# Kernel optimization log

Hardware: AMD Instinct MI355X
Metric: run time of the kernel (lower is better)

## Reference

```python
import jax, jax.numpy as jnp
import numpy as np

V, E, H, B, S = 50000, 512, 1024, 256, 256


def setup_inputs() -> dict:
    key = jax.random.key(0)
    ks = jax.random.split(key, 8)
    inputs = jax.random.randint(ks[0], (B, S), 0, V)
    emb = jax.random.normal(ks[1], (V, E), dtype=jnp.float32)
    sx, sh = 1.0 / np.sqrt(E), 1.0 / np.sqrt(H)  # ~orthogonal column scale
    Wx_f = jax.random.normal(ks[2], (E, 4 * H), dtype=jnp.float32) * sx
    Wh_f = jax.random.normal(ks[3], (H, 4 * H), dtype=jnp.float32) * sh
    Wx_b = jax.random.normal(ks[4], (E, 4 * H), dtype=jnp.float32) * sx
    Wh_b = jax.random.normal(ks[5], (H, 4 * H), dtype=jnp.float32) * sh
    # gate order i, f, o, c ; forget-gate bias initialized to 1 as in the source
    bias = jnp.concatenate([jnp.zeros(H), jnp.ones(H), jnp.zeros(H), jnp.zeros(H)]).astype(jnp.float32)
    W_hq = jax.random.normal(ks[6], (H, 10), dtype=jnp.float32) * sh
    b_q = jnp.zeros(10, dtype=jnp.float32)
    return {"inputs": inputs, "emb": emb, "Wx_f": Wx_f, "Wh_f": Wh_f, "b_f": bias,
            "Wx_b": Wx_b, "Wh_b": Wh_b, "b_b": bias, "W_hq": W_hq, "b_q": b_q}


def _lstm_final_h(x_tbe, Wx, Wh, b):
    """x_tbe: [S,B,E] time-major. Returns final hidden state [B,H]."""
    h0 = jnp.zeros((x_tbe.shape[1], H), dtype=x_tbe.dtype)
    c0 = jnp.zeros_like(h0)

    def cell(carry, X):
        h, c = carry
        g = X @ Wx + h @ Wh + b          # [B, 4H] fused gate pre-activations
        i, f, o, ct = jnp.split(g, 4, axis=-1)
        c = jax.nn.sigmoid(f) * c + jax.nn.sigmoid(i) * jnp.tanh(ct)
        h = jax.nn.sigmoid(o) * jnp.tanh(c)
        return (h, c), None

    (h, _), _ = jax.lax.scan(cell, (h0, c0), x_tbe)
    return h


def reference(inputs, emb, Wx_f, Wh_f, b_f, Wx_b, Wh_b, b_b, W_hq, b_q):
    x = emb[inputs]                      # [B,S,E]
    x = jnp.transpose(x, (1, 0, 2))      # [S,B,E] time-major
    h_fwd = _lstm_final_h(x, Wx_f, Wh_f, b_f)
    h_bwd = _lstm_final_h(x[::-1], Wx_b, Wh_b, b_b)
    logits = (h_fwd + h_bwd) @ W_hq + b_q
    return jax.nn.softmax(logits, axis=1)
```

## Files before the change

kernel.cpp:

```cpp
#include <hip/hip_runtime.h>

#define S_LEN 256
#define BATCH 256
#define EDIM 512
#define HDIM 1024
#define LDS_BYTES 131072

typedef short short8 __attribute__((ext_vector_type(8)));
typedef float f32x4 __attribute__((ext_vector_type(4)));
typedef unsigned long long u64;
typedef unsigned short us;

__device__ __forceinline__ us f2bf(float f) {
  unsigned u = __float_as_uint(f);
  u = u + 0x7FFFu + ((u >> 16) & 1u);
  return (us)(u >> 16);
}
__device__ __forceinline__ float bf2f(us s) {
  return __uint_as_float(((unsigned)s) << 16);
}
__device__ __forceinline__ float sigf(float x) { return 1.0f / (1.0f + __expf(-x)); }
__device__ __forceinline__ float tanh_(float x) { return 2.0f / (1.0f + __expf(-2.0f * x)) - 1.0f; }

#define MFMA(d, a, b) d = __builtin_amdgcn_mfma_f32_16x16x32_bf16(a, b, d, 0, 0, 0)

__device__ __forceinline__ short8 load_hfrag(const us* p) {
  union { u64 d[2]; short8 v; } u;
  u.d[0] = __hip_atomic_load((const u64*)p,       __ATOMIC_RELAXED, __HIP_MEMORY_SCOPE_AGENT);
  u.d[1] = __hip_atomic_load((const u64*)(p + 4), __ATOMIC_RELAXED, __HIP_MEMORY_SCOPE_AGENT);
  return u.v;
}
__device__ __forceinline__ short8 ldf(const us* p) {
  union { uint4 d; short8 v; } u;
  u.d = *(const uint4*)p;
  return u.v;
}


__global__ void gather_embed(const int* __restrict__ inputs, const float* __restrict__ emb,
                             us* __restrict__ Xf) {
  int T = blockIdx.x * 256 + threadIdx.x;
  int kt = T & 15;
  int b  = (T >> 4) & 255;
  int s  = T >> 12;
  int vid = inputs[b * S_LEN + s];
  const float* src = emb + (size_t)vid * EDIM + kt * 32;
  int c = b & 15;
  us* ub = Xf + ((size_t)(s * 16 + kt) * 16 + (b >> 4)) * 512;
#pragma unroll
  for (int q = 0; q < 4; ++q) {
    float4 v0 = *(const float4*)(src + q * 8);
    float4 v1 = *(const float4*)(src + q * 8 + 4);
    us o[8] = { f2bf(v0.x), f2bf(v0.y), f2bf(v0.z), f2bf(v0.w),
                f2bf(v1.x), f2bf(v1.y), f2bf(v1.z), f2bf(v1.w) };
    *(uint4*)(ub + (size_t)(c + 16 * q) * 8) = *(const uint4*)o;
  }
}

__global__ void pack_w(const float* __restrict__ Wx_f, const float* __restrict__ Wh_f,
                       const float* __restrict__ Wx_b, const float* __restrict__ Wh_b,
                       us* __restrict__ Wxp, us* __restrict__ Whp) {
  int T = blockIdx.x * 256 + threadIdx.x;
  int c = T & 15;
  int q = (T >> 4) & 3;
  int t = (T >> 6) & 7;
  int r = T >> 9;
  int kit = r % 48;
  int jbd = r / 48;
  int jb  = jbd & 31;
  int dir = jbd >> 5;
  int g = t >> 1, h16 = t & 1;
  int n = g * 1024 + jb * 32 + h16 * 16 + c;
  const float* W; int k0;
  if (kit < 16) { W = dir ? Wx_b : Wx_f; k0 = kit * 32 + q * 8; }
  else          { W = dir ? Wh_b : Wh_f; k0 = (kit - 16) * 32 + q * 8; }
  us o[8];
#pragma unroll
  for (int e = 0; e < 8; ++e) o[e] = f2bf(W[(size_t)(k0 + e) * 4096 + n]);
  us* dst;
  if (kit < 16) dst = Wxp + (((size_t)(dir * 32 + jb) * 16 + kit) * 8 + t) * 512;
  else          dst = Whp + (((size_t)(dir * 32 + jb) * 32 + (kit - 16)) * 8 + t) * 512;
  *(uint4*)(dst + (size_t)(c + 16 * q) * 8) = *(const uint4*)o;
}

__global__ __launch_bounds__(512, 1) void lstm_main(
    const us* __restrict__ Xf,
    const us* __restrict__ Wxp,
    const us* __restrict__ Whp,
    const float* __restrict__ bias_f,
    const float* __restrict__ bias_b,
    us* __restrict__ Hf,
    unsigned int* __restrict__ slots)
{
  extern __shared__ __align__(16) unsigned char smem[];

  const int bx   = blockIdx.x;
  const int xcd  = bx & 7;
  const int dir  = xcd >> 2;
  const int joct = xcd & 3;
  const int rr   = bx >> 3;
  const int jb   = joct * 8 + (rr & 7);
  const int mq   = rr >> 3;

  const int tid  = threadIdx.x;
  const int wave = tid >> 6;
  const int lane = tid & 63;
  const int mw   = wave & 3;
  const int nw   = wave >> 2;
  const int c    = lane & 15;
  const int q    = lane >> 4;
  const int lofs = lane * 8;

  {
    const uint4* src = (const uint4*)(Whp + (((size_t)(dir * 32 + jb) * 32 + 16) * 8) * 512);
    for (int i = tid; i < 8192; i += 512) *(uint4*)(smem + (size_t)i * 16) = src[i];
  }
  const float* bias = dir ? bias_b : bias_f;
  const int j = jb * 32 + nw * 16 + c;
  float bg[4];
#pragma unroll
  for (int g = 0; g < 4; ++g) bg[g] = bias[g * HDIM + j];
  __syncthreads();

  unsigned int* grp_slots = slots + (dir * 4 + mq) * (32 * 16);
  unsigned int* my_slot   = grp_slots + jb * 16;

  const int bt0 = mq * 4 + mw;
  const us* xu_base  = Xf + (size_t)bt0 * 512 + lofs;
  const us* wxu = Wxp + (((size_t)(dir * 32 + jb) * 16) * 8 + nw) * 512 + lofs;
  const us* whu = Whp + (((size_t)(dir * 32 + jb) * 32) * 8 + nw) * 512 + lofs;
  const int ldsofs = (nw * 512 + lane * 8) * 2;

  float c_reg[4] = {0.f, 0.f, 0.f, 0.f};

  for (int s = 0; s < S_LEN; ++s) {
    const int sx = dir ? (S_LEN - 1 - s) : s;
    const int p  = s & 1;

    f32x4 acc[4];
#pragma unroll
    for (int g = 0; g < 4; ++g)
      acc[g] = (f32x4){bg[g], bg[g], bg[g], bg[g]};

    {
      const us* xu = xu_base + (size_t)sx * (16 * 16 * 512);
#pragma unroll 4
      for (int k = 0; k < 16; ++k) {
        short8 a0 = ldf(xu + (size_t)k * 8192);
        const us* wb = wxu + (size_t)k * 4096;
        short8 b0 = ldf(wb);
        short8 b1 = ldf(wb + 1024);
        short8 b2 = ldf(wb + 2048);
        short8 b3 = ldf(wb + 3072);
        MFMA(acc[0], a0, b0); MFMA(acc[1], a0, b1);
        MFMA(acc[2], a0, b2); MFMA(acc[3], a0, b3);
      }
    }

    if (s > 0) {
      if (tid < 32) {
        const unsigned int* sl = grp_slots + tid * 16;
        for (;;) {
          unsigned v = __hip_atomic_load(sl, __ATOMIC_RELAXED, __HIP_MEMORY_SCOPE_AGENT);
          if (!__any(v < (unsigned)s)) break;
          __builtin_amdgcn_s_sleep(1);
        }
      }
      __syncthreads();
      asm volatile("" ::: "memory");
    }

    {
      const us* hu = Hf + (((size_t)(p * 2 + dir) * 32) * 16 + bt0) * 512 + lofs;
      short8 pa[4];
#pragma unroll
      for (int i = 0; i < 4; ++i) pa[i] = load_hfrag(hu + (size_t)i * 8192);
#pragma unroll 4
      for (int k = 0; k < 16; ++k) {
        short8 a0 = pa[k & 3];
        pa[k & 3] = load_hfrag(hu + (size_t)(k + 4) * 8192);
        const us* wb = whu + (size_t)k * 4096;
        short8 b0 = ldf(wb);
        short8 b1 = ldf(wb + 1024);
        short8 b2 = ldf(wb + 2048);
        short8 b3 = ldf(wb + 3072);
        MFMA(acc[0], a0, b0); MFMA(acc[1], a0, b1);
        MFMA(acc[2], a0, b2); MFMA(acc[3], a0, b3);
      }
#pragma unroll 4
      for (int k = 16; k < 28; ++k) {
        short8 a0 = pa[k & 3];
        pa[k & 3] = load_hfrag(hu + (size_t)(k + 4) * 8192);
        const unsigned char* lb = smem + (size_t)(k - 16) * 8192 + ldsofs;
        short8 b0 = *(const short8*)(lb);
        short8 b1 = *(const short8*)(lb + 2048);
        short8 b2 = *(const short8*)(lb + 4096);
        short8 b3 = *(const short8*)(lb + 6144);
        MFMA(acc[0], a0, b0); MFMA(acc[1], a0, b1);
        MFMA(acc[2], a0, b2); MFMA(acc[3], a0, b3);
      }
#pragma unroll
      for (int k = 28; k < 32; ++k) {
        short8 a0 = pa[k & 3];
        const unsigned char* lb = smem + (size_t)(k - 16) * 8192 + ldsofs;
        short8 b0 = *(const short8*)(lb);
        short8 b1 = *(const short8*)(lb + 2048);
        short8 b2 = *(const short8*)(lb + 4096);
        short8 b3 = *(const short8*)(lb + 6144);
        MFMA(acc[0], a0, b0); MFMA(acc[1], a0, b1);
        MFMA(acc[2], a0, b2); MFMA(acc[3], a0, b3);
      }
    }

    {
      const int q2 = nw * 2 + (c >> 3);
      const int e2 = c & 7;
      const size_t ob = ((size_t)(((p ^ 1) * 2 + dir) * 32 + jb) * 16 + bt0) * 512;
      us* hd = Hf + ob + (size_t)(16 * q2) * 8 + e2;
#pragma unroll
      for (int rg = 0; rg < 4; ++rg) {
        float gi = acc[0][rg], gf = acc[1][rg];
        float go = acc[2][rg], gc = acc[3][rg];
        float cn = sigf(gf) * c_reg[rg] + sigf(gi) * tanh_(gc);
        c_reg[rg] = cn;
        __hip_atomic_store(hd + (size_t)(q * 4 + rg) * 8, f2bf(sigf(go) * tanh_(cn)),
                           __ATOMIC_RELAXED, __HIP_MEMORY_SCOPE_AGENT);
      }
    }
    asm volatile("s_waitcnt vmcnt(0)" ::: "memory");
    __syncthreads();
    if (tid == 0)
      __hip_atomic_store(my_slot, (unsigned)(s + 1), __ATOMIC_RELAXED, __HIP_MEMORY_SCOPE_AGENT);
  }
}

__global__ void final_softmax(const us* __restrict__ Hf,
                              const float* __restrict__ Whq,
                              const float* __restrict__ bq,
                              float* __restrict__ out) {
  __shared__ float red[4][10];
  const int b = blockIdx.x;
  const int tid = threadIdx.x;
  float acc[10];
#pragma unroll
  for (int qq = 0; qq < 10; ++qq) acc[qq] = 0.f;
#pragma unroll
  for (int u = 0; u < 4; ++u) {
    int j = tid * 4 + u;
    int kt = j >> 5, q2 = (j & 31) >> 3, e = j & 7;
    size_t idx = (((size_t)kt * 16 + (b >> 4)) * 512) + ((size_t)((b & 15) + 16 * q2)) * 8 + e;
    float xv = bf2f(Hf[idx]) + bf2f(Hf[(size_t)32 * 16 * 512 + idx]);
#pragma unroll
    for (int qq = 0; qq < 10; ++qq) acc[qq] += xv * Whq[j * 10 + qq];
  }
#pragma unroll
  for (int qq = 0; qq < 10; ++qq)
#pragma unroll
    for (int off = 32; off; off >>= 1) acc[qq] += __shfl_down(acc[qq], off, 64);
  if ((tid & 63) == 0)
#pragma unroll
    for (int qq = 0; qq < 10; ++qq) red[tid >> 6][qq] = acc[qq];
  __syncthreads();
  if (tid == 0) {
    float t[10];
#pragma unroll
    for (int qq = 0; qq < 10; ++qq)
      t[qq] = red[0][qq] + red[1][qq] + red[2][qq] + red[3][qq] + bq[qq];
    float mx = t[0];
#pragma unroll
    for (int qq = 1; qq < 10; ++qq) mx = fmaxf(mx, t[qq]);
    float sum = 0.f;
#pragma unroll
    for (int qq = 0; qq < 10; ++qq) { t[qq] = __expf(t[qq] - mx); sum += t[qq]; }
    float inv = 1.0f / sum;
#pragma unroll
    for (int qq = 0; qq < 10; ++qq) out[b * 10 + qq] = t[qq] * inv;
  }
}

extern "C" void kernel_launch(void* const* d_in, const int* in_sizes, int n_in,
                              void* d_out, int out_size, void* d_ws, size_t ws_size,
                              hipStream_t stream) {
  const int*   inputs = (const int*)d_in[0];
  const float* emb    = (const float*)d_in[1];
  const float* Wx_f   = (const float*)d_in[2];
  const float* Wh_f   = (const float*)d_in[3];
  const float* b_f    = (const float*)d_in[4];
  const float* Wx_b   = (const float*)d_in[5];
  const float* Wh_b   = (const float*)d_in[6];
  const float* b_b    = (const float*)d_in[7];
  const float* W_hq   = (const float*)d_in[8];
  const float* b_q    = (const float*)d_in[9];
  float* out = (float*)d_out;

  char* ws = (char*)d_ws;
  us* Xf  = (us*)ws;
  us* Wxp = (us*)(ws + (64ull << 20));
  us* Whp = (us*)(ws + (72ull << 20));
  us* Hf  = (us*)(ws + (88ull << 20));
  unsigned int* slt = (unsigned int*)(ws + (90ull << 20));

  hipMemsetAsync(Hf, 0, (size_t)2 * 2 * 32 * 16 * 512 * sizeof(us), stream);
  hipMemsetAsync(slt, 0, 8 * 32 * 16 * sizeof(unsigned int), stream);

  gather_embed<<<4096, 256, 0, stream>>>(inputs, emb, Xf);
  pack_w<<<6144, 256, 0, stream>>>(Wx_f, Wh_f, Wx_b, Wh_b, Wxp, Whp);

  hipFuncSetAttribute((const void*)lstm_main,
                      hipFuncAttributeMaxDynamicSharedMemorySize, LDS_BYTES);

  const us* xf_p = Xf;
  const us* wxp_p = Wxp;
  const us* whp_p = Whp;
  const float* bf_p = b_f;
  const float* bb_p = b_b;
  us* hf_p = Hf;
  unsigned int* slt_p = slt;
  void* kargs[] = { (void*)&xf_p, (void*)&wxp_p, (void*)&whp_p, (void*)&bf_p,
                    (void*)&bb_p, (void*)&hf_p, (void*)&slt_p };
  hipLaunchCooperativeKernel((void*)lstm_main, dim3(256), dim3(512), kargs, LDS_BYTES, stream);

  final_softmax<<<256, 256, 0, stream>>>(Hf, W_hq, b_q, out);
}
```

Measured before the change: 4.714 ms.

## Repartition LSTM blocks so each block's whole recurrent weight slice fits in LDS

Result: no change. 4.714 ms (-0.0%).

```diff
diff --git a/kernel.cpp b/kernel.cpp
--- a/kernel.cpp
+++ b/kernel.cpp
@@ -94,42 +94,44 @@
 {
   extern __shared__ __align__(16) unsigned char smem[];
 
-  const int bx   = blockIdx.x;
-  const int xcd  = bx & 7;
-  const int dir  = xcd >> 2;
-  const int joct = xcd & 3;
-  const int rr   = bx >> 3;
-  const int jb   = joct * 8 + (rr & 7);
-  const int mq   = rr >> 3;
+  const int bx  = blockIdx.x;
+  const int dir = bx & 1;
+  const int mq  = (bx >> 1) & 1;
+  const int J   = bx >> 2;
+  const int jh  = J & 1;
+  const int jt  = J >> 1;
 
   const int tid  = threadIdx.x;
   const int wave = tid >> 6;
   const int lane = tid & 63;
-  const int mw   = wave & 3;
-  const int nw   = wave >> 2;
   const int c    = lane & 15;
   const int q    = lane >> 4;
   const int lofs = lane * 8;
 
   {
-    const uint4* src = (const uint4*)(Whp + (((size_t)(dir * 32 + jb) * 32 + 16) * 8) * 512);
-    for (int i = tid; i < 8192; i += 512) *(uint4*)(smem + (size_t)i * 16) = src[i];
+    const uint4* W4 = (const uint4*)Whp;
+    for (int i = tid; i < 8192; i += 512) {
+      int within = i & 63;
+      int g  = (i >> 6) & 3;
+      int hk = i >> 8;
+      size_t src = ((((size_t)(dir * 32 + jt) * 32 + hk) * 8) + (g * 2 + jh)) * 64 + within;
+      *(uint4*)(smem + (size_t)i * 16) = W4[src];
+    }
   }
   const float* bias = dir ? bias_b : bias_f;
-  const int j = jb * 32 + nw * 16 + c;
+  const int j = J * 16 + c;
   float bg[4];
 #pragma unroll
   for (int g = 0; g < 4; ++g) bg[g] = bias[g * HDIM + j];
   __syncthreads();
 
-  unsigned int* grp_slots = slots + (dir * 4 + mq) * (32 * 16);
-  unsigned int* my_slot   = grp_slots + jb * 16;
-
-  const int bt0 = mq * 4 + mw;
-  const us* xu_base  = Xf + (size_t)bt0 * 512 + lofs;
-  const us* wxu = Wxp + (((size_t)(dir * 32 + jb) * 16) * 8 + nw) * 512 + lofs;
-  const us* whu = Whp + (((size_t)(dir * 32 + jb) * 32) * 8 + nw) * 512 + lofs;
-  const int ldsofs = (nw * 512 + lane * 8) * 2;
+  unsigned int* grp_slots = slots + (dir * 2 + mq) * (64 * 16);
+  unsigned int* my_slot   = grp_slots + J * 16;
+
+  const int bt0 = mq * 8 + wave;
+  const us* xu_base = Xf + (size_t)bt0 * 512 + lofs;
+  const us* wxu = Wxp + ((size_t)(dir * 32 + jt) * 16) * 8 * 512 + (size_t)jh * 512 + lofs;
+  const unsigned char* lbbase = smem + (size_t)lane * 16;
 
   float c_reg[4] = {0.f, 0.f, 0.f, 0.f};
 
@@ -158,7 +160,7 @@
     }
 
     if (s > 0) {
-      if (tid < 32) {
+      if (tid < 64) {
         const unsigned int* sl = grp_slots + tid * 16;
         for (;;) {
           unsigned v = __hip_atomic_load(sl, __ATOMIC_RELAXED, __HIP_MEMORY_SCOPE_AGENT);
@@ -176,46 +178,34 @@
 #pragma unroll
       for (int i = 0; i < 4; ++i) pa[i] = load_hfrag(hu + (size_t)i * 8192);
 #pragma unroll 4
-      for (int k = 0; k < 16; ++k) {
+      for (int k = 0; k < 28; ++k) {
         short8 a0 = pa[k & 3];
         pa[k & 3] = load_hfrag(hu + (size_t)(k + 4) * 8192);
-        const us* wb = whu + (size_t)k * 4096;
-        short8 b0 = ldf(wb);
-        short8 b1 = ldf(wb + 1024);
-        short8 b2 = ldf(wb + 2048);
-        short8 b3 = ldf(wb + 3072);
+        const unsigned char* lb = lbbase + (size_t)k * 4096;
+        short8 b0 = *(const short8*)(lb);
+        short8 b1 = *(const short8*)(lb + 1024);
+        short8 b2 = *(const short8*)(lb + 2048);
+        short8 b3 = *(const short8*)(lb + 3072);
         MFMA(acc[0], a0, b0); MFMA(acc[1], a0, b1);
         MFMA(acc[2], a0, b2); MFMA(acc[3], a0, b3);
       }
-#pragma unroll 4
-      for (int k = 16; k < 28; ++k) {
+#pragma unroll
+      for (int k = 28; k < 32; ++k) {
         short8 a0 = pa[k & 3];
-        pa[k & 3] = load_hfrag(hu + (size_t)(k + 4) * 8192);
-        const unsigned char* lb = smem + (size_t)(k - 16) * 8192 + ldsofs;
+        const unsigned char* lb = lbbase + (size_t)k * 4096;
         short8 b0 = *(const short8*)(lb);
-        short8 b1 = *(const short8*)(lb + 2048);
-        short8 b2 = *(const short8*)(lb + 4096);
-        short8 b3 = *(const short8*)(lb + 6144);
+        short8 b1 = *(const short8*)(lb + 1024);
+        short8 b2 = *(const short8*)(lb + 2048);
+        short8 b3 = *(const short8*)(lb + 3072);
         MFMA(acc[0], a0, b0); MFMA(acc[1], a0, b1);
         MFMA(acc[2], a0, b2); MFMA(acc[3], a0, b3);
       }
-#pragma unroll
-      for (int k = 28; k < 32; ++k) {
-        short8 a0 = pa[k & 3];
-        const unsigned char* lb = smem + (size_t)(k - 16) * 8192 + ldsofs;
-        short8 b0 = *(const short8*)(lb);
-        short8 b1 = *(const short8*)(lb + 2048);
-        short8 b2 = *(const short8*)(lb + 4096);
-        short8 b3 = *(const short8*)(lb + 6144);
-        MFMA(acc[0], a0, b0); MFMA(acc[1], a0, b1);
-        MFMA(acc[2], a0, b2); MFMA(acc[3], a0, b3);
-      }
     }
 
     {
-      const int q2 = nw * 2 + (c >> 3);
+      const int q2 = jh * 2 + (c >> 3);
       const int e2 = c & 7;
-      const size_t ob = ((size_t)(((p ^ 1) * 2 + dir) * 32 + jb) * 16 + bt0) * 512;
+      const size_t ob = ((size_t)(((p ^ 1) * 2 + dir) * 32 + jt) * 16 + bt0) * 512;
       us* hd = Hf + ob + (size_t)(16 * q2) * 8 + e2;
 #pragma unroll
       for (int rg = 0; rg < 4; ++rg) {
@@ -301,7 +291,7 @@
   unsigned int* slt = (unsigned int*)(ws + (90ull << 20));
 
   hipMemsetAsync(Hf, 0, (size_t)2 * 2 * 32 * 16 * 512 * sizeof(us), stream);
-  hipMemsetAsync(slt, 0, 8 * 32 * 16 * sizeof(unsigned int), stream);
+  hipMemsetAsync(slt, 0, 4 * 64 * 16 * sizeof(unsigned int), stream);
 
   gather_embed<<<4096, 256, 0, stream>>>(inputs, emb, Xf);
   pack_w<<<6144, 256, 0, stream>>>(Wx_f, Wh_f, Wx_b, Wh_b, Wxp, Whp);
```
